# Kernel optimization log

Hardware: AMD Instinct MI355X
Metric: run time of the kernel (lower is better)

## Reference

```python
import jax, jax.numpy as jnp
import numpy as np

B, N, C = 16, 25200, 80      # batch, anchors (YOLOv5@640), COCO classes
T_MAX = 50                   # max targets per image
MAX_DET = 300                # NMS candidate cap (static output size)
CONF_THRES = 0.8
NMS_THRES = 0.4


def cxcywh_to_xyxy(b):
    # cxcywh -> xywh -> xyxy, as in tensor_to_dict
    cx, cy, w, h = b[..., 0], b[..., 1], b[..., 2], b[..., 3]
    half_w, half_h = w * 0.5, h * 0.5
    return jnp.stack([cx - half_w, cy - half_h, cx + half_w, cy + half_h], axis=-1)


def iou_matrix(b):
    # b: [K,4] xyxy -> [K,K] pairwise IoU
    area = (b[:, 2] - b[:, 0]) * (b[:, 3] - b[:, 1])
    lt = jnp.maximum(b[:, None, :2], b[None, :, :2])
    rb = jnp.minimum(b[:, None, 2:], b[None, :, 2:])
    wh = jnp.clip(rb - lt, 0.0)
    inter = wh[..., 0] * wh[..., 1]
    return inter / (area[:, None] + area[None, :] - inter + 1e-9)


def nms_keep(boxes, valid):
    # boxes sorted by score desc; greedy NMS -> bool keep mask [K]
    K = boxes.shape[0]
    iou = iou_matrix(boxes)
    idx = jnp.arange(K)

    def body(i, keep):
        k = keep[i]  # survivor & valid
        suppress = k & (iou[i] > NMS_THRES) & (idx > i)
        return keep & ~suppress

    return jax.lax.fori_loop(0, K, body, valid)


def post_process(logits):
    # logits: [B, N, 4+1+C]
    boxes = cxcywh_to_xyxy(logits[..., :4])          # [B,N,4]
    obj = logits[..., 4]                             # [B,N]
    cls = logits[..., 5:]                            # [B,N,C]
    cls_conf = jnp.max(cls, axis=-1)
    labels = jnp.argmax(cls, axis=-1)
    conf = obj * cls_conf                            # [B,N]
    score = jnp.where(conf > CONF_THRES, conf, -jnp.inf)
    top_s, top_i = jax.lax.top_k(score, MAX_DET)     # [B,K]
    bb = jnp.take_along_axis(boxes, top_i[..., None], axis=1)   # [B,K,4]
    lb = jnp.take_along_axis(labels, top_i, axis=1)             # [B,K]
    valid = top_s > CONF_THRES
    scores = jnp.where(valid, top_s, 0.0)
    keep = jax.vmap(nms_keep)(bb, valid)             # [B,K]
    return bb, scores, lb.astype(jnp.int32), keep


def setup_inputs() -> dict:
    key = jax.random.key(0)
    k1, k2, k3 = jax.random.split(key, 3)
    logits = jax.random.uniform(k1, (B, N, 5 + C), dtype=jnp.float32)
    targets = jax.random.uniform(k2, (B, T_MAX, 6), dtype=jnp.float32)
    target_lengths = jax.random.randint(k3, (B,), 1, T_MAX, dtype=jnp.int64)
    return {"logits": logits, "targets": targets, "target_lengths": target_lengths}


def reference(logits, targets, target_lengths):
    pred_boxes, pred_scores, pred_labels, pred_keep = post_process(logits)
    # targets: ragged slice expressed as a validity mask (jit-static shapes)
    tgt_valid = jnp.arange(T_MAX)[None, :] < target_lengths[:, None]   # [B,T]
    tgt_boxes = cxcywh_to_xyxy(targets[..., :4])                       # [B,T,4]
    tgt_scores = targets[..., 4]
    tgt_labels = targets[..., 5].astype(jnp.int32)                     # labels.shape[1]==1 branch
    return (pred_boxes, pred_scores, pred_labels, pred_keep,
            tgt_boxes, tgt_scores, tgt_labels, tgt_valid)
```

## Files before the change

### kernel.cpp

```cpp
#include <hip/hip_runtime.h>
#include <stdint.h>

#define BATCH   16
#define NANCH   25200
#define NCLS    80
#define REC     85
#define MAXDET  300
#define TMAX    50
#define NBUCKET 2048
#define FIN     512
#define WREG    400
#define RSTRIDE 12
#define SUPW    (MAXDET*RSTRIDE)

#define OFF_PB 0
#define OFF_PS 19200
#define OFF_PL 24000
#define OFF_PK 28800
#define OFF_TB 33600
#define OFF_TS 36800
#define OFF_TL 37600
#define OFF_TV 38400

__device__ __forceinline__ float opaque_f(float x) { asm volatile("" : "+v"(x)); return x; }

__global__ __launch_bounds__(256) void kA(const float* __restrict__ logits,
                                          unsigned* __restrict__ confout,
                                          unsigned* __restrict__ labout) {
    const int wid  = (blockIdx.x * 256 + threadIdx.x) >> 6;
    const int lane = threadIdx.x & 63;
    const int t    = lane >> 2;
    const int j    = lane & 3;
    const int a    = wid * 16 + t;
    const float obj = logits[(size_t)a * REC + 4];
    unsigned cf = 0u;
    if (obj > 0.8f) {
        const float* cls = logits + (size_t)a * REC + 5 + j * 20;
        float v[20];
#pragma unroll
        for (int i = 0; i < 5; ++i) {
            float4 q = *(const float4*)(cls + 4 * i);
            v[4*i+0] = q.x; v[4*i+1] = q.y; v[4*i+2] = q.z; v[4*i+3] = q.w;
        }
        float m = v[0];
#pragma unroll
        for (int i = 1; i < 20; ++i) m = fmaxf(m, v[i]);
        m = fmaxf(m, __shfl_xor(m, 1));
        m = fmaxf(m, __shfl_xor(m, 2));
        int lc = 255;
#pragma unroll
        for (int i = 0; i < 20; ++i) lc = min(lc, (v[i] == m) ? (j * 20 + i) : 255);
        lc = min(lc, __shfl_xor(lc, 1));
        lc = min(lc, __shfl_xor(lc, 2));
        const float conf = obj * m;
        cf = (conf > 0.8f) ? __float_as_uint(conf) : 0u;
        if (j == 0) labout[a] = (unsigned)lc;
    }
    if (j == 0) confout[a] = cf;
}

__global__ __launch_bounds__(1024) void kSel(const float* __restrict__ logits,
                                             const unsigned* __restrict__ confbits,
                                             const unsigned* __restrict__ labels,
                                             const float* __restrict__ targets,
                                             const int* __restrict__ tlen,
                                             float* __restrict__ out) {
    __shared__ unsigned long long cand[16 * WREG];
    __shared__ unsigned hist[NBUCKET];
    __shared__ unsigned long long fin[FIN];
    __shared__ unsigned long long srt[MAXDET];
    __shared__ int wcnts[16];
    __shared__ int sTb, sCnt;
    const int b = blockIdx.x;
    const int tid = threadIdx.x;
    const int lane = tid & 63;
    const int w = tid >> 6;

    if (tid >= 512 && tid < 512 + TMAX) {
        int t = tid - 512;
        bool is64 = (tlen[1] == 0) && (tlen[3] == 0) && (tlen[5] == 0);
        int len = is64 ? tlen[2 * b] : tlen[b];
        const float* r = targets + ((size_t)b * TMAX + t) * 6;
        float cx = r[0], cy = r[1], wd = r[2], h = r[3], sc = r[4], lb = r[5];
        float hw = opaque_f(wd * 0.5f);
        float hh = opaque_f(h * 0.5f);
        size_t o = (size_t)b * TMAX + t;
        out[OFF_TB + o * 4 + 0] = cx - hw;
        out[OFF_TB + o * 4 + 1] = cy - hh;
        out[OFF_TB + o * 4 + 2] = cx + hw;
        out[OFF_TB + o * 4 + 3] = cy + hh;
        out[OFF_TS + o] = sc;
        out[OFF_TL + o] = (float)(int)lb;
        out[OFF_TV + o] = (t < len) ? 1.0f : 0.0f;
    }

    for (int i = tid; i < NBUCKET; i += 1024) hist[i] = 0u;
    if (tid < MAXDET) srt[tid] = 0ull;
    if (tid == 0) sCnt = 0;
    __syncthreads();

    const uint4* cb4 = (const uint4*)(confbits + (size_t)b * NANCH);
    int wcnt = 0;
    for (int i = tid; i < NANCH / 4; i += 1024) {
        uint4 u = cb4[i];
        unsigned wsv[4] = {u.x, u.y, u.z, u.w};
#pragma unroll
        for (int c = 0; c < 4; ++c) {
            unsigned bits = wsv[c];
            bool pass = (bits != 0u);
            unsigned long long mk = __ballot(pass);
            if (pass) {
                int p = wcnt + __popcll(mk & ((1ull << lane) - 1ull));
                if (p < WREG)
                    cand[w * WREG + p] = ((unsigned long long)bits << 32) |
                                         (unsigned)(0xFFFFFFFFu - (unsigned)(i * 4 + c));
            }
            wcnt += (int)__popcll(mk);
        }
    }
    if (lane == 0 && w < 16) wcnts[w] = (wcnt < WREG) ? wcnt : WREG;
    __syncthreads();

    for (int s = tid; s < 16 * WREG; s += 1024) {
        int rw = s / WREG, idx = s - rw * WREG;
        if (idx < wcnts[rw]) {
            unsigned bits = (unsigned)(cand[s] >> 32);
            unsigned bk = (bits - 0x3F4CCCCDu) >> 11;
            if (bk > NBUCKET - 1u) bk = NBUCKET - 1u;
            atomicAdd(&hist[bk], 1u);
        }
    }
    __syncthreads();

    if (tid < 64) {
        const int l = tid;
        unsigned sup = 0u;
        for (int j = 0; j < 32; ++j) sup += hist[l * 32 + j];
        unsigned ss = sup;
        for (int off = 1; off < 64; off <<= 1) {
            unsigned v = __shfl_down(ss, off);
            ss += (l + off < 64) ? v : 0u;
        }
        bool ge = ss >= MAXDET;
        unsigned long long mask = __ballot(ge);
        int sstar = (mask == 0ull) ? 0 : (63 - __clzll(mask));
        unsigned tail = (sstar < 63) ? __shfl(ss, sstar + 1) : 0u;
        unsigned h = (l < 32) ? hist[sstar * 32 + l] : 0u;
        unsigned s2 = h;
        for (int off = 1; off < 32; off <<= 1) {
            unsigned v = __shfl_down(s2, off);
            s2 += (l + off < 32) ? v : 0u;
        }
        bool ge2 = (l < 32) && (s2 + tail >= MAXDET);
        unsigned long long m2 = __ballot(ge2);
        int lstar = (m2 == 0ull) ? 0 : (63 - __clzll(m2));
        if (l == 0) sTb = sstar * 32 + lstar;
    }
    __syncthreads();

    const int tb = sTb;
    for (int s = tid; s < 16 * WREG; s += 1024) {
        int rw = s / WREG, idx = s - rw * WREG;
        bool pass = false;
        unsigned long long k = 0ull;
        if (idx < wcnts[rw]) {
            k = cand[s];
            unsigned bits = (unsigned)(k >> 32);
            unsigned bk = (bits - 0x3F4CCCCDu) >> 11;
            if (bk > NBUCKET - 1u) bk = NBUCKET - 1u;
            pass = ((int)bk >= tb);
        }
        unsigned long long mk = __ballot(pass);
        if (mk) {
            int base = 0;
            if (lane == 0) base = atomicAdd(&sCnt, (int)__popcll(mk));
            base = __shfl(base, 0);
            if (pass) {
                int p = base + __popcll(mk & ((1ull << lane) - 1ull));
                if (p < FIN) fin[p] = k;
            }
        }
    }
    __syncthreads();
    const int fc = (sCnt < FIN) ? sCnt : FIN;

    if (tid < fc) {
        unsigned long long k = fin[tid];
        int r = 0;
        for (int j = 0; j < fc; ++j) r += (fin[j] > k) ? 1 : 0;
        if (r < MAXDET) srt[r] = k;
    }
    __syncthreads();

    if (tid < MAXDET) {
        unsigned long long key = srt[tid];
        float score = __uint_as_float((unsigned)(key >> 32));
        unsigned n = 0xFFFFFFFFu - (unsigned)(key & 0xFFFFFFFFull);
        if (n >= NANCH) n = 0;
        const size_t ga = (size_t)b * NANCH + n;
        float4 bq = *(const float4*)(logits + ga * REC);
        unsigned lab = labels[ga];
        float hw = opaque_f(bq.z * 0.5f);
        float hh = opaque_f(bq.w * 0.5f);
        float x1 = bq.x - hw, y1 = bq.y - hh, x2 = bq.x + hw, y2 = bq.y + hh;
        size_t o = (size_t)(b * MAXDET + tid);
        out[OFF_PB + o * 4 + 0] = x1;
        out[OFF_PB + o * 4 + 1] = y1;
        out[OFF_PB + o * 4 + 2] = x2;
        out[OFF_PB + o * 4 + 3] = y2;
        out[OFF_PS + o] = score;
        out[OFF_PL + o] = (float)lab;
    }
}

__global__ __launch_bounds__(256) void kSup(const float* __restrict__ out,
                                            unsigned* __restrict__ suppg) {
    __shared__ float4 sb[MAXDET];
    __shared__ float sar[MAXDET];
    const int b = blockIdx.x >> 3;
    const int s = blockIdx.x & 7;
    const int tid = threadIdx.x;
    const int lane = tid & 63;
    const int w = tid >> 6;
    const float4* boxes = (const float4*)(out + OFF_PB) + (size_t)b * MAXDET;
    for (int t = tid; t < MAXDET; t += 256) {
        float4 q = boxes[t];
        sb[t] = q;
        sar[t] = (q.z - q.x) * (q.w - q.y);
    }
    __syncthreads();
    const int i0 = s * 38;
    const int i1 = min(i0 + 38, MAXDET);
    unsigned* sg = suppg + (size_t)b * SUPW;
    for (int i = i0 + w; i < i1; i += 4) {
        float4 bi = sb[i];
        float ai = sar[i];
#pragma unroll
        for (int c = 0; c < 5; ++c) {
            int j = c * 64 + lane;
            bool pass = false;
            if (j < MAXDET && j > i) {
                float4 bj = sb[j];
                float aj = sar[j];
                float ltx = fmaxf(bi.x, bj.x);
                float lty = fmaxf(bi.y, bj.y);
                float rbx = fminf(bi.z, bj.z);
                float rby = fminf(bi.w, bj.w);
                float wx = fmaxf(rbx - ltx, 0.0f);
                float wy = fmaxf(rby - lty, 0.0f);
                float inter = wx * wy;
                float iou = inter / (ai + aj - inter + 1e-9f);
                pass = (iou > 0.4f);
            }
            unsigned long long mk = __ballot(pass);
            if (lane == 0)  sg[i * RSTRIDE + 2 * c]     = ~(unsigned)mk;
            if (lane == 32) sg[i * RSTRIDE + 2 * c + 1] = ~(unsigned)(mk >> 32);
        }
    }
}

#define PROC(C, KWC)                                                   \
    {                                                                  \
        unsigned todo = KWC;                                           \
        while (todo) {                                                 \
            int i2 = __ffs(todo) - 1;                                  \
            const uint4 a  = s4[(C * 32 + i2) * 3 + 0];                \
            const uint4 bq = s4[(C * 32 + i2) * 3 + 1];                \
            const uint4 cq = s4[(C * 32 + i2) * 3 + 2];                \
            kw0 &= a.x;  kw1 &= a.y;  kw2 &= a.z;  kw3 &= a.w;         \
            kw4 &= bq.x; kw5 &= bq.y; kw6 &= bq.z; kw7 &= bq.w;        \
            kw8 &= cq.x; kw9 &= cq.y;                                  \
            unsigned long long done = ((unsigned long long)2 << i2) - 1ull; \
            todo = KWC & ~(unsigned)done;                              \
        }                                                              \
    }

__global__ __launch_bounds__(512) void kScan(const unsigned* __restrict__ suppg,
                                             float* __restrict__ out) {
    __shared__ __align__(16) unsigned supp[SUPW];
    __shared__ unsigned keepw[10];
    const int b = blockIdx.x;
    const int tid = threadIdx.x;
    const uint4* g4 = (const uint4*)(suppg + (size_t)b * SUPW);
    uint4* l4 = (uint4*)supp;
    for (int t = tid; t < SUPW / 4; t += 512) l4[t] = g4[t];
    __syncthreads();
    if (tid < 64) {
        const uint4* s4 = (const uint4*)supp;
        unsigned kw0 = ~0u, kw1 = ~0u, kw2 = ~0u, kw3 = ~0u, kw4 = ~0u;
        unsigned kw5 = ~0u, kw6 = ~0u, kw7 = ~0u, kw8 = ~0u, kw9 = 0xFFFu;
        PROC(0, kw0) PROC(1, kw1) PROC(2, kw2) PROC(3, kw3) PROC(4, kw4)
        PROC(5, kw5) PROC(6, kw6) PROC(7, kw7) PROC(8, kw8) PROC(9, kw9)
        if (tid == 0) {
            keepw[0] = kw0; keepw[1] = kw1; keepw[2] = kw2; keepw[3] = kw3;
            keepw[4] = kw4; keepw[5] = kw5; keepw[6] = kw6; keepw[7] = kw7;
            keepw[8] = kw8; keepw[9] = kw9;
        }
    }
    __syncthreads();
    if (tid < MAXDET)
        out[OFF_PK + (size_t)b * MAXDET + tid] =
            ((keepw[tid >> 5] >> (tid & 31)) & 1u) ? 1.0f : 0.0f;
}

extern "C" void kernel_launch(void* const* d_in, const int* in_sizes, int n_in,
                              void* d_out, int out_size, void* d_ws, size_t ws_size,
                              hipStream_t stream) {
    const float* logits  = (const float*)d_in[0];
    const float* targets = (const float*)d_in[1];
    const int*   tlen    = (const int*)d_in[2];
    float* out = (float*)d_out;
    char* ws = (char*)d_ws;
    unsigned* confbits = (unsigned*)ws;
    unsigned* labels   = (unsigned*)(ws + (size_t)BATCH * NANCH * 4);
    unsigned* suppg    = (unsigned*)(ws + (size_t)BATCH * NANCH * 8);

    hipLaunchKernelGGL(kA, dim3(6300), dim3(256), 0, stream, logits, confbits, labels);
    hipLaunchKernelGGL(kSel, dim3(BATCH), dim3(1024), 0, stream,
                       logits, confbits, labels, targets, tlen, out);
    hipLaunchKernelGGL(kSup, dim3(BATCH * 8), dim3(256), 0, stream, out, suppg);
    hipLaunchKernelGGL(kScan, dim3(BATCH), dim3(512), 0, stream, suppg, out);
}
```

Baseline: 58.03 us.

## Fuse NMS into selection kernel with on-the-fly IoU in greedy scan

Removes the separate suppression-matrix and scan kernels. After top-K selection, boxes and areas stay in shared memory, and a single wavefront runs the greedy scan, computing IoU rows only for surviving boxes via ballot. This saves two launches and the global round trip of the suppression matrix. In exchange, the IoU work is serialized on one wave per image instead of being spread across 128 blocks.

```diff
diff --git a/kernel.cpp b/kernel.cpp
--- a/kernel.cpp
+++ b/kernel.cpp
@@ -10,8 +10,6 @@
 #define NBUCKET 2048
 #define FIN     512
 #define WREG    400
-#define RSTRIDE 12
-#define SUPW    (MAXDET*RSTRIDE)
 
 #define OFF_PB 0
 #define OFF_PS 19200
@@ -59,6 +57,47 @@
     if (j == 0) confout[a] = cf;
 }
 
+#define NMS_ROW(i, C2, KWA, KWB)                                          \
+    {                                                                     \
+        const float4 bi = sbox[i];                                        \
+        const float  ai = sarr[i];                                        \
+        {                                                                 \
+            int j = (C2) * 64 + lane;                                     \
+            bool pass = false;                                            \
+            if (j < MAXDET && j > (i)) {                                  \
+                float4 bj = sbox[j];                                      \
+                float aj = sarr[j];                                       \
+                float ltx = fmaxf(bi.x, bj.x);                            \
+                float lty = fmaxf(bi.y, bj.y);                            \
+                float rbx = fminf(bi.z, bj.z);                            \
+                float rby = fminf(bi.w, bj.w);                            \
+                float wx = fmaxf(rbx - ltx, 0.0f);                        \
+                float wy = fmaxf(rby - lty, 0.0f);                        \
+                float inter = wx * wy;                                    \
+                float iou = inter / (ai + aj - inter + 1e-9f);            \
+                pass = (iou > 0.4f);                                      \
+            }                                                             \
+            unsigned long long mk = __ballot(pass);                       \
+            KWA &= ~(unsigned)mk;                                         \
+            KWB &= ~(unsigned)(mk >> 32);                                 \
+        }                                                                 \
+    }
+
+#define NMS_ALLROWS(i)                                                    \
+    NMS_ROW(i, 0, kw0, kw1) NMS_ROW(i, 1, kw2, kw3) NMS_ROW(i, 2, kw4, kw5) \
+    NMS_ROW(i, 3, kw6, kw7) NMS_ROW(i, 4, kw8, kw9)
+
+#define PROC(C, KWC)                                                      \
+    {                                                                     \
+        unsigned todo = KWC;                                              \
+        while (todo) {                                                    \
+            int i2 = __ffs(todo) - 1;                                     \
+            NMS_ALLROWS(C * 32 + i2)                                      \
+            unsigned long long done = ((unsigned long long)2 << i2) - 1ull; \
+            todo = KWC & ~(unsigned)done;                                 \
+        }                                                                 \
+    }
+
 __global__ __launch_bounds__(1024) void kSel(const float* __restrict__ logits,
                                              const unsigned* __restrict__ confbits,
                                              const unsigned* __restrict__ labels,
@@ -69,6 +108,9 @@
     __shared__ unsigned hist[NBUCKET];
     __shared__ unsigned long long fin[FIN];
     __shared__ unsigned long long srt[MAXDET];
+    __shared__ float4 sbox[MAXDET];
+    __shared__ float  sarr[MAXDET];
+    __shared__ unsigned keepw[10];
     __shared__ int wcnts[16];
     __shared__ int sTb, sCnt;
     const int b = blockIdx.x;
@@ -203,6 +245,8 @@
         float hw = opaque_f(bq.z * 0.5f);
         float hh = opaque_f(bq.w * 0.5f);
         float x1 = bq.x - hw, y1 = bq.y - hh, x2 = bq.x + hw, y2 = bq.y + hh;
+        sbox[tid] = make_float4(x1, y1, x2, y2);
+        sarr[tid] = (x2 - x1) * (y2 - y1);
         size_t o = (size_t)(b * MAXDET + tid);
         out[OFF_PB + o * 4 + 0] = x1;
         out[OFF_PB + o * 4 + 1] = y1;
@@ -211,82 +255,9 @@
         out[OFF_PS + o] = score;
         out[OFF_PL + o] = (float)lab;
     }
-}
-
-__global__ __launch_bounds__(256) void kSup(const float* __restrict__ out,
-                                            unsigned* __restrict__ suppg) {
-    __shared__ float4 sb[MAXDET];
-    __shared__ float sar[MAXDET];
-    const int b = blockIdx.x >> 3;
-    const int s = blockIdx.x & 7;
-    const int tid = threadIdx.x;
-    const int lane = tid & 63;
-    const int w = tid >> 6;
-    const float4* boxes = (const float4*)(out + OFF_PB) + (size_t)b * MAXDET;
-    for (int t = tid; t < MAXDET; t += 256) {
-        float4 q = boxes[t];
-        sb[t] = q;
-        sar[t] = (q.z - q.x) * (q.w - q.y);
-    }
-    __syncthreads();
-    const int i0 = s * 38;
-    const int i1 = min(i0 + 38, MAXDET);
-    unsigned* sg = suppg + (size_t)b * SUPW;
-    for (int i = i0 + w; i < i1; i += 4) {
-        float4 bi = sb[i];
-        float ai = sar[i];
-#pragma unroll
-        for (int c = 0; c < 5; ++c) {
-            int j = c * 64 + lane;
-            bool pass = false;
-            if (j < MAXDET && j > i) {
-                float4 bj = sb[j];
-                float aj = sar[j];
-                float ltx = fmaxf(bi.x, bj.x);
-                float lty = fmaxf(bi.y, bj.y);
-                float rbx = fminf(bi.z, bj.z);
-                float rby = fminf(bi.w, bj.w);
-                float wx = fmaxf(rbx - ltx, 0.0f);
-                float wy = fmaxf(rby - lty, 0.0f);
-                float inter = wx * wy;
-                float iou = inter / (ai + aj - inter + 1e-9f);
-                pass = (iou > 0.4f);
-            }
-            unsigned long long mk = __ballot(pass);
-            if (lane == 0)  sg[i * RSTRIDE + 2 * c]     = ~(unsigned)mk;
-            if (lane == 32) sg[i * RSTRIDE + 2 * c + 1] = ~(unsigned)(mk >> 32);
-        }
-    }
-}
-
-#define PROC(C, KWC)                                                   \
-    {                                                                  \
-        unsigned todo = KWC;                                           \
-        while (todo) {                                                 \
-            int i2 = __ffs(todo) - 1;                                  \
-            const uint4 a  = s4[(C * 32 + i2) * 3 + 0];                \
-            const uint4 bq = s4[(C * 32 + i2) * 3 + 1];                \
-            const uint4 cq = s4[(C * 32 + i2) * 3 + 2];                \
-            kw0 &= a.x;  kw1 &= a.y;  kw2 &= a.z;  kw3 &= a.w;         \
-            kw4 &= bq.x; kw5 &= bq.y; kw6 &= bq.z; kw7 &= bq.w;        \
-            kw8 &= cq.x; kw9 &= cq.y;                                  \
-            unsigned long long done = ((unsigned long long)2 << i2) - 1ull; \
-            todo = KWC & ~(unsigned)done;                              \
-        }                                                              \
-    }
-
-__global__ __launch_bounds__(512) void kScan(const unsigned* __restrict__ suppg,
-                                             float* __restrict__ out) {
-    __shared__ __align__(16) unsigned supp[SUPW];
-    __shared__ unsigned keepw[10];
-    const int b = blockIdx.x;
-    const int tid = threadIdx.x;
-    const uint4* g4 = (const uint4*)(suppg + (size_t)b * SUPW);
-    uint4* l4 = (uint4*)supp;
-    for (int t = tid; t < SUPW / 4; t += 512) l4[t] = g4[t];
-    __syncthreads();
+    __syncthreads();
+
     if (tid < 64) {
-        const uint4* s4 = (const uint4*)supp;
         unsigned kw0 = ~0u, kw1 = ~0u, kw2 = ~0u, kw3 = ~0u, kw4 = ~0u;
         unsigned kw5 = ~0u, kw6 = ~0u, kw7 = ~0u, kw8 = ~0u, kw9 = 0xFFFu;
         PROC(0, kw0) PROC(1, kw1) PROC(2, kw2) PROC(3, kw3) PROC(4, kw4)
@@ -313,11 +284,8 @@
     char* ws = (char*)d_ws;
     unsigned* confbits = (unsigned*)ws;
     unsigned* labels   = (unsigned*)(ws + (size_t)BATCH * NANCH * 4);
-    unsigned* suppg    = (unsigned*)(ws + (size_t)BATCH * NANCH * 8);
 
     hipLaunchKernelGGL(kA, dim3(6300), dim3(256), 0, stream, logits, confbits, labels);
     hipLaunchKernelGGL(kSel, dim3(BATCH), dim3(1024), 0, stream,
                        logits, confbits, labels, targets, tlen, out);
-    hipLaunchKernelGGL(kSup, dim3(BATCH * 8), dim3(256), 0, stream, out, suppg);
-    hipLaunchKernelGGL(kScan, dim3(BATCH), dim3(512), 0, stream, suppg, out);
 }
```

Result: slower. 79.22 us (+36.5%).

## Merge selection, IoU and scan kernels into one cooperative kernel with grid syncs

Applied to the files above, without the earlier changes.

Replaces the three kernels after kA (kSel, kSup, kScan) with one cooperative kernel of 128 blocks that uses grid.sync between phases. Candidate compaction is now split across 8 blocks per image, writing fragments to global memory, instead of running on one 1024-thread block per image. Histogram threshold selection, sorting and the keep scan still run on one block per image. This removes two kernel launch gaps and spreads the confbits scan, at the cost of three grid-wide barriers and a global-memory round trip for the fragments.

```diff
diff --git a/kernel.cpp b/kernel.cpp
--- a/kernel.cpp
+++ b/kernel.cpp
@@ -1,5 +1,8 @@
 #include <hip/hip_runtime.h>
+#include <hip/hip_cooperative_groups.h>
 #include <stdint.h>
+
+namespace cg = cooperative_groups;
 
 #define BATCH   16
 #define NANCH   25200
@@ -9,7 +12,7 @@
 #define TMAX    50
 #define NBUCKET 2048
 #define FIN     512
-#define WREG    400
+#define FRAGCAP 800
 #define RSTRIDE 12
 #define SUPW    (MAXDET*RSTRIDE)
 
@@ -57,206 +60,6 @@
         if (j == 0) labout[a] = (unsigned)lc;
     }
     if (j == 0) confout[a] = cf;
-}
-
-__global__ __launch_bounds__(1024) void kSel(const float* __restrict__ logits,
-                                             const unsigned* __restrict__ confbits,
-                                             const unsigned* __restrict__ labels,
-                                             const float* __restrict__ targets,
-                                             const int* __restrict__ tlen,
-                                             float* __restrict__ out) {
-    __shared__ unsigned long long cand[16 * WREG];
-    __shared__ unsigned hist[NBUCKET];
-    __shared__ unsigned long long fin[FIN];
-    __shared__ unsigned long long srt[MAXDET];
-    __shared__ int wcnts[16];
-    __shared__ int sTb, sCnt;
-    const int b = blockIdx.x;
-    const int tid = threadIdx.x;
-    const int lane = tid & 63;
-    const int w = tid >> 6;
-
-    if (tid >= 512 && tid < 512 + TMAX) {
-        int t = tid - 512;
-        bool is64 = (tlen[1] == 0) && (tlen[3] == 0) && (tlen[5] == 0);
-        int len = is64 ? tlen[2 * b] : tlen[b];
-        const float* r = targets + ((size_t)b * TMAX + t) * 6;
-        float cx = r[0], cy = r[1], wd = r[2], h = r[3], sc = r[4], lb = r[5];
-        float hw = opaque_f(wd * 0.5f);
-        float hh = opaque_f(h * 0.5f);
-        size_t o = (size_t)b * TMAX + t;
-        out[OFF_TB + o * 4 + 0] = cx - hw;
-        out[OFF_TB + o * 4 + 1] = cy - hh;
-        out[OFF_TB + o * 4 + 2] = cx + hw;
-        out[OFF_TB + o * 4 + 3] = cy + hh;
-        out[OFF_TS + o] = sc;
-        out[OFF_TL + o] = (float)(int)lb;
-        out[OFF_TV + o] = (t < len) ? 1.0f : 0.0f;
-    }
-
-    for (int i = tid; i < NBUCKET; i += 1024) hist[i] = 0u;
-    if (tid < MAXDET) srt[tid] = 0ull;
-    if (tid == 0) sCnt = 0;
-    __syncthreads();
-
-    const uint4* cb4 = (const uint4*)(confbits + (size_t)b * NANCH);
-    int wcnt = 0;
-    for (int i = tid; i < NANCH / 4; i += 1024) {
-        uint4 u = cb4[i];
-        unsigned wsv[4] = {u.x, u.y, u.z, u.w};
-#pragma unroll
-        for (int c = 0; c < 4; ++c) {
-            unsigned bits = wsv[c];
-            bool pass = (bits != 0u);
-            unsigned long long mk = __ballot(pass);
-            if (pass) {
-                int p = wcnt + __popcll(mk & ((1ull << lane) - 1ull));
-                if (p < WREG)
-                    cand[w * WREG + p] = ((unsigned long long)bits << 32) |
-                                         (unsigned)(0xFFFFFFFFu - (unsigned)(i * 4 + c));
-            }
-            wcnt += (int)__popcll(mk);
-        }
-    }
-    if (lane == 0 && w < 16) wcnts[w] = (wcnt < WREG) ? wcnt : WREG;
-    __syncthreads();
-
-    for (int s = tid; s < 16 * WREG; s += 1024) {
-        int rw = s / WREG, idx = s - rw * WREG;
-        if (idx < wcnts[rw]) {
-            unsigned bits = (unsigned)(cand[s] >> 32);
-            unsigned bk = (bits - 0x3F4CCCCDu) >> 11;
-            if (bk > NBUCKET - 1u) bk = NBUCKET - 1u;
-            atomicAdd(&hist[bk], 1u);
-        }
-    }
-    __syncthreads();
-
-    if (tid < 64) {
-        const int l = tid;
-        unsigned sup = 0u;
-        for (int j = 0; j < 32; ++j) sup += hist[l * 32 + j];
-        unsigned ss = sup;
-        for (int off = 1; off < 64; off <<= 1) {
-            unsigned v = __shfl_down(ss, off);
-            ss += (l + off < 64) ? v : 0u;
-        }
-        bool ge = ss >= MAXDET;
-        unsigned long long mask = __ballot(ge);
-        int sstar = (mask == 0ull) ? 0 : (63 - __clzll(mask));
-        unsigned tail = (sstar < 63) ? __shfl(ss, sstar + 1) : 0u;
-        unsigned h = (l < 32) ? hist[sstar * 32 + l] : 0u;
-        unsigned s2 = h;
-        for (int off = 1; off < 32; off <<= 1) {
-            unsigned v = __shfl_down(s2, off);
-            s2 += (l + off < 32) ? v : 0u;
-        }
-        bool ge2 = (l < 32) && (s2 + tail >= MAXDET);
-        unsigned long long m2 = __ballot(ge2);
-        int lstar = (m2 == 0ull) ? 0 : (63 - __clzll(m2));
-        if (l == 0) sTb = sstar * 32 + lstar;
-    }
-    __syncthreads();
-
-    const int tb = sTb;
-    for (int s = tid; s < 16 * WREG; s += 1024) {
-        int rw = s / WREG, idx = s - rw * WREG;
-        bool pass = false;
-        unsigned long long k = 0ull;
-        if (idx < wcnts[rw]) {
-            k = cand[s];
-            unsigned bits = (unsigned)(k >> 32);
-            unsigned bk = (bits - 0x3F4CCCCDu) >> 11;
-            if (bk > NBUCKET - 1u) bk = NBUCKET - 1u;
-            pass = ((int)bk >= tb);
-        }
-        unsigned long long mk = __ballot(pass);
-        if (mk) {
-            int base = 0;
-            if (lane == 0) base = atomicAdd(&sCnt, (int)__popcll(mk));
-            base = __shfl(base, 0);
-            if (pass) {
-                int p = base + __popcll(mk & ((1ull << lane) - 1ull));
-                if (p < FIN) fin[p] = k;
-            }
-        }
-    }
-    __syncthreads();
-    const int fc = (sCnt < FIN) ? sCnt : FIN;
-
-    if (tid < fc) {
-        unsigned long long k = fin[tid];
-        int r = 0;
-        for (int j = 0; j < fc; ++j) r += (fin[j] > k) ? 1 : 0;
-        if (r < MAXDET) srt[r] = k;
-    }
-    __syncthreads();
-
-    if (tid < MAXDET) {
-        unsigned long long key = srt[tid];
-        float score = __uint_as_float((unsigned)(key >> 32));
-        unsigned n = 0xFFFFFFFFu - (unsigned)(key & 0xFFFFFFFFull);
-        if (n >= NANCH) n = 0;
-        const size_t ga = (size_t)b * NANCH + n;
-        float4 bq = *(const float4*)(logits + ga * REC);
-        unsigned lab = labels[ga];
-        float hw = opaque_f(bq.z * 0.5f);
-        float hh = opaque_f(bq.w * 0.5f);
-        float x1 = bq.x - hw, y1 = bq.y - hh, x2 = bq.x + hw, y2 = bq.y + hh;
-        size_t o = (size_t)(b * MAXDET + tid);
-        out[OFF_PB + o * 4 + 0] = x1;
-        out[OFF_PB + o * 4 + 1] = y1;
-        out[OFF_PB + o * 4 + 2] = x2;
-        out[OFF_PB + o * 4 + 3] = y2;
-        out[OFF_PS + o] = score;
-        out[OFF_PL + o] = (float)lab;
-    }
-}
-
-__global__ __launch_bounds__(256) void kSup(const float* __restrict__ out,
-                                            unsigned* __restrict__ suppg) {
-    __shared__ float4 sb[MAXDET];
-    __shared__ float sar[MAXDET];
-    const int b = blockIdx.x >> 3;
-    const int s = blockIdx.x & 7;
-    const int tid = threadIdx.x;
-    const int lane = tid & 63;
-    const int w = tid >> 6;
-    const float4* boxes = (const float4*)(out + OFF_PB) + (size_t)b * MAXDET;
-    for (int t = tid; t < MAXDET; t += 256) {
-        float4 q = boxes[t];
-        sb[t] = q;
-        sar[t] = (q.z - q.x) * (q.w - q.y);
-    }
-    __syncthreads();
-    const int i0 = s * 38;
-    const int i1 = min(i0 + 38, MAXDET);
-    unsigned* sg = suppg + (size_t)b * SUPW;
-    for (int i = i0 + w; i < i1; i += 4) {
-        float4 bi = sb[i];
-        float ai = sar[i];
-#pragma unroll
-        for (int c = 0; c < 5; ++c) {
-            int j = c * 64 + lane;
-            bool pass = false;
-            if (j < MAXDET && j > i) {
-                float4 bj = sb[j];
-                float aj = sar[j];
-                float ltx = fmaxf(bi.x, bj.x);
-                float lty = fmaxf(bi.y, bj.y);
-                float rbx = fminf(bi.z, bj.z);
-                float rby = fminf(bi.w, bj.w);
-                float wx = fmaxf(rbx - ltx, 0.0f);
-                float wy = fmaxf(rby - lty, 0.0f);
-                float inter = wx * wy;
-                float iou = inter / (ai + aj - inter + 1e-9f);
-                pass = (iou > 0.4f);
-            }
-            unsigned long long mk = __ballot(pass);
-            if (lane == 0)  sg[i * RSTRIDE + 2 * c]     = ~(unsigned)mk;
-            if (lane == 32) sg[i * RSTRIDE + 2 * c + 1] = ~(unsigned)(mk >> 32);
-        }
-    }
 }
 
 #define PROC(C, KWC)                                                   \
@@ -275,32 +78,240 @@
         }                                                              \
     }
 
-__global__ __launch_bounds__(512) void kScan(const unsigned* __restrict__ suppg,
-                                             float* __restrict__ out) {
+__global__ __launch_bounds__(256, 1) void kCoop(const float* __restrict__ logits,
+                                                const unsigned* __restrict__ confbits,
+                                                const unsigned* __restrict__ labels,
+                                                unsigned long long* __restrict__ fragg,
+                                                int* __restrict__ cntg,
+                                                unsigned* __restrict__ suppg,
+                                                const float* __restrict__ targets,
+                                                const int* __restrict__ tlen,
+                                                float* __restrict__ out) {
+    cg::grid_group grid = cg::this_grid();
+    __shared__ unsigned hist[NBUCKET];
+    __shared__ unsigned long long fin[FIN];
+    __shared__ unsigned long long srt[MAXDET];
+    __shared__ float4 sb[MAXDET];
+    __shared__ float  sar[MAXDET];
     __shared__ __align__(16) unsigned supp[SUPW];
     __shared__ unsigned keepw[10];
-    const int b = blockIdx.x;
+    __shared__ int scnt, sTb;
+    const int blk = blockIdx.x;
+    const int b = blk >> 3;
+    const int s = blk & 7;
     const int tid = threadIdx.x;
-    const uint4* g4 = (const uint4*)(suppg + (size_t)b * SUPW);
-    uint4* l4 = (uint4*)supp;
-    for (int t = tid; t < SUPW / 4; t += 512) l4[t] = g4[t];
+    const int lane = tid & 63;
+    const int w = tid >> 6;
+
+    if (tid == 0) scnt = 0;
     __syncthreads();
-    if (tid < 64) {
-        const uint4* s4 = (const uint4*)supp;
-        unsigned kw0 = ~0u, kw1 = ~0u, kw2 = ~0u, kw3 = ~0u, kw4 = ~0u;
-        unsigned kw5 = ~0u, kw6 = ~0u, kw7 = ~0u, kw8 = ~0u, kw9 = 0xFFFu;
-        PROC(0, kw0) PROC(1, kw1) PROC(2, kw2) PROC(3, kw3) PROC(4, kw4)
-        PROC(5, kw5) PROC(6, kw6) PROC(7, kw7) PROC(8, kw8) PROC(9, kw9)
-        if (tid == 0) {
-            keepw[0] = kw0; keepw[1] = kw1; keepw[2] = kw2; keepw[3] = kw3;
-            keepw[4] = kw4; keepw[5] = kw5; keepw[6] = kw6; keepw[7] = kw7;
-            keepw[8] = kw8; keepw[9] = kw9;
-        }
-    }
-    __syncthreads();
-    if (tid < MAXDET)
-        out[OFF_PK + (size_t)b * MAXDET + tid] =
-            ((keepw[tid >> 5] >> (tid & 31)) & 1u) ? 1.0f : 0.0f;
+    {
+        const uint4* cb4 = (const uint4*)(confbits + (size_t)b * NANCH);
+        const int u40 = s * 788;
+        const int u41 = min(6300, u40 + 788);
+        unsigned long long* fg = fragg + (size_t)(b * 8 + s) * FRAGCAP;
+        for (int i = u40 + tid; i < u41; i += 256) {
+            uint4 u = cb4[i];
+            unsigned arr[4] = {u.x, u.y, u.z, u.w};
+#pragma unroll
+            for (int c = 0; c < 4; ++c) {
+                unsigned bits = arr[c];
+                bool pass = (bits != 0u);
+                unsigned long long mk = __ballot(pass);
+                if (mk) {
+                    int base = 0;
+                    if (lane == 0) base = atomicAdd(&scnt, (int)__popcll(mk));
+                    base = __shfl(base, 0);
+                    if (pass) {
+                        int p = base + __popcll(mk & ((1ull << lane) - 1ull));
+                        if (p < FRAGCAP)
+                            fg[p] = ((unsigned long long)bits << 32) |
+                                    (unsigned)(0xFFFFFFFFu - (unsigned)(i * 4 + c));
+                    }
+                }
+            }
+        }
+        __syncthreads();
+        if (tid == 0) cntg[b * 8 + s] = (scnt < FRAGCAP) ? scnt : FRAGCAP;
+    }
+    __threadfence();
+    grid.sync();
+
+    if (s == 0) {
+        for (int i = tid; i < NBUCKET; i += 256) hist[i] = 0u;
+        for (int i = tid; i < MAXDET; i += 256) srt[i] = 0ull;
+        if (tid == 0) scnt = 0;
+        __syncthreads();
+        for (int st = 0; st < 8; ++st) {
+            int c = cntg[b * 8 + st];
+            const unsigned long long* f = fragg + (size_t)(b * 8 + st) * FRAGCAP;
+            for (int i = tid; i < c; i += 256) {
+                unsigned bits = (unsigned)(f[i] >> 32);
+                unsigned bk = (bits - 0x3F4CCCCDu) >> 11;
+                if (bk > NBUCKET - 1u) bk = NBUCKET - 1u;
+                atomicAdd(&hist[bk], 1u);
+            }
+        }
+        __syncthreads();
+        if (tid < 64) {
+            const int l = tid;
+            unsigned sup = 0u;
+            for (int j = 0; j < 32; ++j) sup += hist[l * 32 + j];
+            unsigned ss = sup;
+            for (int off = 1; off < 64; off <<= 1) {
+                unsigned v = __shfl_down(ss, off);
+                ss += (l + off < 64) ? v : 0u;
+            }
+            bool ge = ss >= MAXDET;
+            unsigned long long mask = __ballot(ge);
+            int sstar = (mask == 0ull) ? 0 : (63 - __clzll(mask));
+            unsigned tail = (sstar < 63) ? __shfl(ss, sstar + 1) : 0u;
+            unsigned h = (l < 32) ? hist[sstar * 32 + l] : 0u;
+            unsigned s2 = h;
+            for (int off = 1; off < 32; off <<= 1) {
+                unsigned v = __shfl_down(s2, off);
+                s2 += (l + off < 32) ? v : 0u;
+            }
+            bool ge2 = (l < 32) && (s2 + tail >= MAXDET);
+            unsigned long long m2 = __ballot(ge2);
+            int lstar = (m2 == 0ull) ? 0 : (63 - __clzll(m2));
+            if (l == 0) sTb = sstar * 32 + lstar;
+        }
+        __syncthreads();
+        const int tb = sTb;
+        for (int st = 0; st < 8; ++st) {
+            int c = cntg[b * 8 + st];
+            const unsigned long long* f = fragg + (size_t)(b * 8 + st) * FRAGCAP;
+            for (int i = tid; i < c; i += 256) {
+                unsigned long long k = f[i];
+                unsigned bits = (unsigned)(k >> 32);
+                unsigned bk = (bits - 0x3F4CCCCDu) >> 11;
+                if (bk > NBUCKET - 1u) bk = NBUCKET - 1u;
+                bool pass = ((int)bk >= tb);
+                unsigned long long mk = __ballot(pass);
+                if (mk) {
+                    int base = 0;
+                    if (lane == 0) base = atomicAdd(&scnt, (int)__popcll(mk));
+                    base = __shfl(base, 0);
+                    if (pass) {
+                        int p = base + __popcll(mk & ((1ull << lane) - 1ull));
+                        if (p < FIN) fin[p] = k;
+                    }
+                }
+            }
+        }
+        __syncthreads();
+        const int fc = (scnt < FIN) ? scnt : FIN;
+        for (int i = tid; i < fc; i += 256) {
+            unsigned long long k = fin[i];
+            int r = 0;
+            for (int j = 0; j < fc; ++j) r += (fin[j] > k) ? 1 : 0;
+            if (r < MAXDET) srt[r] = k;
+        }
+        __syncthreads();
+        for (int i = tid; i < MAXDET; i += 256) {
+            unsigned long long key = srt[i];
+            float score = __uint_as_float((unsigned)(key >> 32));
+            unsigned n = 0xFFFFFFFFu - (unsigned)(key & 0xFFFFFFFFull);
+            if (n >= NANCH) n = 0;
+            const size_t ga = (size_t)b * NANCH + n;
+            float4 bq = *(const float4*)(logits + ga * REC);
+            unsigned lab = labels[ga];
+            float hw = opaque_f(bq.z * 0.5f);
+            float hh = opaque_f(bq.w * 0.5f);
+            float x1 = bq.x - hw, y1 = bq.y - hh, x2 = bq.x + hw, y2 = bq.y + hh;
+            size_t o = (size_t)(b * MAXDET + i);
+            out[OFF_PB + o * 4 + 0] = x1;
+            out[OFF_PB + o * 4 + 1] = y1;
+            out[OFF_PB + o * 4 + 2] = x2;
+            out[OFF_PB + o * 4 + 3] = y2;
+            out[OFF_PS + o] = score;
+            out[OFF_PL + o] = (float)lab;
+        }
+    } else if (s == 1) {
+        if (tid < TMAX) {
+            int t = tid;
+            bool is64 = (tlen[1] == 0) && (tlen[3] == 0) && (tlen[5] == 0);
+            int len = is64 ? tlen[2 * b] : tlen[b];
+            const float* r = targets + ((size_t)b * TMAX + t) * 6;
+            float cx = r[0], cy = r[1], wd = r[2], h = r[3], sc = r[4], lb = r[5];
+            float hw = opaque_f(wd * 0.5f);
+            float hh = opaque_f(h * 0.5f);
+            size_t o = (size_t)b * TMAX + t;
+            out[OFF_TB + o * 4 + 0] = cx - hw;
+            out[OFF_TB + o * 4 + 1] = cy - hh;
+            out[OFF_TB + o * 4 + 2] = cx + hw;
+            out[OFF_TB + o * 4 + 3] = cy + hh;
+            out[OFF_TS + o] = sc;
+            out[OFF_TL + o] = (float)(int)lb;
+            out[OFF_TV + o] = (t < len) ? 1.0f : 0.0f;
+        }
+    }
+    __threadfence();
+    grid.sync();
+
+    {
+        const float4* boxes = (const float4*)(out + OFF_PB) + (size_t)b * MAXDET;
+        for (int t = tid; t < MAXDET; t += 256) {
+            float4 q = boxes[t];
+            sb[t] = q;
+            sar[t] = (q.z - q.x) * (q.w - q.y);
+        }
+        __syncthreads();
+        const int i0 = s * 38;
+        const int i1 = min(i0 + 38, MAXDET);
+        unsigned* sg = suppg + (size_t)b * SUPW;
+        for (int i = i0 + w; i < i1; i += 4) {
+            float4 bi = sb[i];
+            float ai = sar[i];
+#pragma unroll
+            for (int c = 0; c < 5; ++c) {
+                int j = c * 64 + lane;
+                bool pass = false;
+                if (j < MAXDET && j > i) {
+                    float4 bj = sb[j];
+                    float aj = sar[j];
+                    float ltx = fmaxf(bi.x, bj.x);
+                    float lty = fmaxf(bi.y, bj.y);
+                    float rbx = fminf(bi.z, bj.z);
+                    float rby = fminf(bi.w, bj.w);
+                    float wx = fmaxf(rbx - ltx, 0.0f);
+                    float wy = fmaxf(rby - lty, 0.0f);
+                    float inter = wx * wy;
+                    float iou = inter / (ai + aj - inter + 1e-9f);
+                    pass = (iou > 0.4f);
+                }
+                unsigned long long mk = __ballot(pass);
+                if (lane == 0)  sg[i * RSTRIDE + 2 * c]     = ~(unsigned)mk;
+                if (lane == 32) sg[i * RSTRIDE + 2 * c + 1] = ~(unsigned)(mk >> 32);
+            }
+        }
+    }
+    __threadfence();
+    grid.sync();
+
+    if (s == 0) {
+        const uint4* g4 = (const uint4*)(suppg + (size_t)b * SUPW);
+        uint4* l4 = (uint4*)supp;
+        for (int t = tid; t < SUPW / 4; t += 256) l4[t] = g4[t];
+        __syncthreads();
+        if (tid < 64) {
+            const uint4* s4 = (const uint4*)supp;
+            unsigned kw0 = ~0u, kw1 = ~0u, kw2 = ~0u, kw3 = ~0u, kw4 = ~0u;
+            unsigned kw5 = ~0u, kw6 = ~0u, kw7 = ~0u, kw8 = ~0u, kw9 = 0xFFFu;
+            PROC(0, kw0) PROC(1, kw1) PROC(2, kw2) PROC(3, kw3) PROC(4, kw4)
+            PROC(5, kw5) PROC(6, kw6) PROC(7, kw7) PROC(8, kw8) PROC(9, kw9)
+            if (tid == 0) {
+                keepw[0] = kw0; keepw[1] = kw1; keepw[2] = kw2; keepw[3] = kw3;
+                keepw[4] = kw4; keepw[5] = kw5; keepw[6] = kw6; keepw[7] = kw7;
+                keepw[8] = kw8; keepw[9] = kw9;
+            }
+        }
+        __syncthreads();
+        for (int i = tid; i < MAXDET; i += 256)
+            out[OFF_PK + (size_t)b * MAXDET + i] =
+                ((keepw[i >> 5] >> (i & 31)) & 1u) ? 1.0f : 0.0f;
+    }
 }
 
 extern "C" void kernel_launch(void* const* d_in, const int* in_sizes, int n_in,
@@ -312,12 +323,15 @@
     float* out = (float*)d_out;
     char* ws = (char*)d_ws;
     unsigned* confbits = (unsigned*)ws;
-    unsigned* labels   = (unsigned*)(ws + (size_t)BATCH * NANCH * 4);
-    unsigned* suppg    = (unsigned*)(ws + (size_t)BATCH * NANCH * 8);
+    unsigned* labels   = (unsigned*)(ws + 1612800);
+    unsigned long long* fragg = (unsigned long long*)(ws + 3225600);
+    int* cntg          = (int*)(ws + 3225600 + 819200);
+    unsigned* suppg    = (unsigned*)(ws + 3225600 + 819200 + 512);
 
     hipLaunchKernelGGL(kA, dim3(6300), dim3(256), 0, stream, logits, confbits, labels);
-    hipLaunchKernelGGL(kSel, dim3(BATCH), dim3(1024), 0, stream,
-                       logits, confbits, labels, targets, tlen, out);
-    hipLaunchKernelGGL(kSup, dim3(BATCH * 8), dim3(256), 0, stream, out, suppg);
-    hipLaunchKernelGGL(kScan, dim3(BATCH), dim3(512), 0, stream, suppg, out);
+
+    void* args[] = {(void*)&logits, (void*)&confbits, (void*)&labels,
+                    (void*)&fragg, (void*)&cntg, (void*)&suppg,
+                    (void*)&targets, (void*)&tlen, (void*)&out};
+    hipLaunchCooperativeKernel((void*)kCoop, dim3(128), dim3(256), args, 0, stream);
 }
```

Result: slower. 145.8 us (+151.3%).
